# Optimization experiments

Hardware: AMD Instinct MI355X
Metric: run time of the kernel (lower is better)

Reference implementation:

```python
import jax, jax.numpy as jnp
import numpy as np

B, S, D, H, HD = 1, 2048, 1024, 16, 64
E, K, F = 8, 2, 2048
Z_COEF, LB_COEF = 0.001, 0.01


def setup_inputs() -> dict:
    key = jax.random.key(0)
    ks = jax.random.split(key, 10)
    s_d = 1.0 / np.sqrt(D)
    s_f = 1.0 / np.sqrt(F)
    return {
        'hidden_states': jax.random.normal(ks[0], (B, S, D), jnp.float32),
        'attention_mask': jnp.tril(jnp.ones((S, S), bool))[None, None],  # causal [1,1,S,S]
        'position_ids': jnp.broadcast_to(jnp.arange(S), (B, S)),
        'ln1_w': jnp.ones((D,), jnp.float32), 'ln1_b': jnp.zeros((D,), jnp.float32),
        'ln2_w': jnp.ones((D,), jnp.float32), 'ln2_b': jnp.zeros((D,), jnp.float32),
        'wq': jax.random.normal(ks[1], (D, D), jnp.float32) * s_d,
        'wk': jax.random.normal(ks[2], (D, D), jnp.float32) * s_d,
        'wv': jax.random.normal(ks[3], (D, D), jnp.float32) * s_d,
        'wo': jax.random.normal(ks[4], (D, D), jnp.float32) * s_d,
        'w_router': jax.random.normal(ks[5], (D, E), jnp.float32) * s_d,
        'w_gate': jax.random.normal(ks[6], (E, D, F), jnp.float32) * s_d,
        'w_up': jax.random.normal(ks[7], (E, D, F), jnp.float32) * s_d,
        'w_down': jax.random.normal(ks[8], (E, F, D), jnp.float32) * s_f,
    }


def _layernorm(x, w, b):
    m = x.mean(-1, keepdims=True)
    v = jnp.mean(jnp.square(x - m), -1, keepdims=True)
    return (x - m) / jnp.sqrt(v + 1e-5) * w + b


def _rotate_half(x):
    x1, x2 = jnp.split(x, 2, axis=-1)
    return jnp.concatenate([-x2, x1], axis=-1)


def _forward(hs, mask, pos, l1w, l1b, l2w, l2b, wq, wk, wv, wo, wr, wg, wu, wd):
    b, s, d = hs.shape
    # --- attention sub-block ---
    res = hs
    x = _layernorm(hs, l1w, l1b)
    q = (x @ wq).reshape(b, s, H, HD).transpose(0, 2, 1, 3)  # [b,H,s,hd]
    k = (x @ wk).reshape(b, s, H, HD).transpose(0, 2, 1, 3)
    v = (x @ wv).reshape(b, s, H, HD).transpose(0, 2, 1, 3)
    inv_freq = 1.0 / (10000.0 ** (jnp.arange(0, HD, 2, dtype=jnp.float32) / HD))
    freqs = pos[..., None].astype(jnp.float32) * inv_freq  # [b,s,hd/2]
    cos = jnp.cos(freqs); sin = jnp.sin(freqs)
    cos = jnp.concatenate([cos, cos], -1)[:, None]  # [b,1,s,hd]
    sin = jnp.concatenate([sin, sin], -1)[:, None]
    q = q * cos + _rotate_half(q) * sin
    k = k * cos + _rotate_half(k) * sin
    scores = jnp.einsum('bhqd,bhkd->bhqk', q, k) / np.sqrt(HD)
    scores = jnp.where(mask, scores, jnp.asarray(-1e9, scores.dtype))
    attn_w = jax.nn.softmax(scores, axis=-1)
    a = jnp.einsum('bhqk,bhkd->bhqd', attn_w, v)
    a = a.transpose(0, 2, 1, 3).reshape(b, s, d)
    hs = res + a @ wo
    # --- MoE sub-block ---
    res = hs
    x = _layernorm(hs, l2w, l2b)
    xt = x.reshape(-1, d)  # [T,D]
    logits = xt @ wr  # [T,E]
    probs = jax.nn.softmax(logits.astype(jnp.float32), axis=-1)
    ew, ei = jax.lax.top_k(probs, K)  # [T,K]
    ew = ew / ew.sum(-1, keepdims=True)
    one_hot = jax.nn.one_hot(ei, E, dtype=jnp.float32)  # [T,K,E]
    combine = jnp.sum(one_hot * ew[..., None], axis=1).astype(xt.dtype)  # [T,E]
    g = jnp.einsum('td,edf->etf', xt, wg)
    u = jnp.einsum('td,edf->etf', xt, wu)
    y = jnp.einsum('etf,efd->etd', jax.nn.silu(g) * u, wd)  # [E,T,D]
    moe_out = jnp.einsum('te,etd->td', combine, y).reshape(b, s, d)
    # --- aux losses ---
    z_loss = Z_COEF * jnp.mean(jnp.square(jax.scipy.special.logsumexp(logits, axis=-1)))
    expert_mask = jnp.sum(one_hot, axis=1)  # [T,E] in {0,1}
    util = expert_mask.sum(0) / (b * s)
    lb_loss = LB_COEF * jnp.sum(util * probs.mean(0))
    aux = z_loss + lb_loss
    return res + moe_out, aux


def reference(hidden_states, attention_mask, position_ids, ln1_w, ln1_b, ln2_w, ln2_b,
              wq, wk, wv, wo, w_router, w_gate, w_up, w_down):
    return _forward(hidden_states, attention_mask, position_ids, ln1_w, ln1_b, ln2_w, ln2_b,
                    wq, wk, wv, wo, w_router, w_gate, w_up, w_down)
```

## Files before the change

### kernel.cpp

```cpp
#include <hip/hip_runtime.h>
#include <math.h>

static constexpr int S = 2048;
static constexpr int D = 1024;
static constexpr int H = 16;
static constexpr int HD = 64;
static constexpr int E = 8;
static constexpr int F = 2048;
static constexpr int NSLOTS = S * 2;
static constexpr int NPAD = NSLOTS + 128;

typedef __attribute__((ext_vector_type(8))) short bf16x8;
typedef __attribute__((ext_vector_type(4))) float f32x4;

__device__ __forceinline__ float bf2f(ushort u) {
    uint32_t x = ((uint32_t)u) << 16; float f; __builtin_memcpy(&f, &x, 4); return f;
}
__device__ __forceinline__ ushort f2bf(float f) {
    uint32_t x; __builtin_memcpy(&x, &f, 4);
    return (ushort)((x + 0x7fffu + ((x >> 16) & 1u)) >> 16);
}
__device__ __forceinline__ void async_copy16(const void* gptr, void* ldsptr) {
    __builtin_amdgcn_global_load_lds(
        (const __attribute__((address_space(1))) void*)gptr,
        (__attribute__((address_space(3))) void*)ldsptr, 16, 0, 0);
}

__global__ __launch_bounds__(256) void castT_kernel(const float* __restrict__ src,
    ushort* __restrict__ dst, int K, int N)
{
    __shared__ float T[64][65];
    int z = blockIdx.z;
    src += (size_t)z * K * N; dst += (size_t)z * K * N;
    int k0 = blockIdx.y * 64, n0 = blockIdx.x * 64;
    int t = threadIdx.x;
    int r = t >> 4, c4 = (t & 15) * 4;
#pragma unroll
    for (int it = 0; it < 4; it++) {
        float4 v = *(const float4*)(src + (size_t)(k0 + r + it * 16) * N + n0 + c4);
        T[r + it * 16][c4 + 0] = v.x; T[r + it * 16][c4 + 1] = v.y;
        T[r + it * 16][c4 + 2] = v.z; T[r + it * 16][c4 + 3] = v.w;
    }
    __syncthreads();
#pragma unroll
    for (int it = 0; it < 4; it++) {
        int rr = r + it * 16;
        ushort4 o;
        o.x = f2bf(T[c4 + 0][rr]); o.y = f2bf(T[c4 + 1][rr]);
        o.z = f2bf(T[c4 + 2][rr]); o.w = f2bf(T[c4 + 3][rr]);
        *(ushort4*)(dst + (size_t)(n0 + rr) * K + k0 + c4) = o;
    }
}

__global__ __launch_bounds__(256) void castT2_kernel(const float* __restrict__ src,
    ushort* __restrict__ dh, ushort* __restrict__ dl, int K, int N)
{
    __shared__ float T[64][65];
    src += (size_t)blockIdx.z * K * N;
    dh += (size_t)blockIdx.z * K * N; dl += (size_t)blockIdx.z * K * N;
    int k0 = blockIdx.y * 64, n0 = blockIdx.x * 64;
    int t = threadIdx.x;
    int r = t >> 4, c4 = (t & 15) * 4;
#pragma unroll
    for (int it = 0; it < 4; it++) {
        float4 v = *(const float4*)(src + (size_t)(k0 + r + it * 16) * N + n0 + c4);
        T[r + it * 16][c4 + 0] = v.x; T[r + it * 16][c4 + 1] = v.y;
        T[r + it * 16][c4 + 2] = v.z; T[r + it * 16][c4 + 3] = v.w;
    }
    __syncthreads();
#pragma unroll
    for (int it = 0; it < 4; it++) {
        int rr = r + it * 16;
        ushort4 oh, ol;
        float v0 = T[c4 + 0][rr], v1 = T[c4 + 1][rr], v2 = T[c4 + 2][rr], v3 = T[c4 + 3][rr];
        oh.x = f2bf(v0); ol.x = f2bf(v0 - bf2f(oh.x));
        oh.y = f2bf(v1); ol.y = f2bf(v1 - bf2f(oh.y));
        oh.z = f2bf(v2); ol.z = f2bf(v2 - bf2f(oh.z));
        oh.w = f2bf(v3); ol.w = f2bf(v3 - bf2f(oh.w));
        *(ushort4*)(dh + (size_t)(n0 + rr) * K + k0 + c4) = oh;
        *(ushort4*)(dl + (size_t)(n0 + rr) * K + k0 + c4) = ol;
    }
}

__global__ __launch_bounds__(256) void ln_kernel(const float* __restrict__ x,
    const float* __restrict__ w, const float* __restrict__ b,
    float* __restrict__ yf, ushort* __restrict__ yh, ushort* __restrict__ yl)
{
    int t = blockIdx.x, tid = threadIdx.x;
    __shared__ float redx[256];
    __shared__ float redy[256];
    const float* xr = x + (size_t)t * D;
    float4 xv = *(const float4*)(xr + tid * 4);
    redx[tid] = xv.x + xv.y + xv.z + xv.w;
    redy[tid] = xv.x * xv.x + xv.y * xv.y + xv.z * xv.z + xv.w * xv.w;
    __syncthreads();
    for (int st = 128; st > 0; st >>= 1) {
        if (tid < st) { redx[tid] += redx[tid + st]; redy[tid] += redy[tid + st]; }
        __syncthreads();
    }
    float mean = redx[0] * (1.0f / D);
    float var  = redy[0] * (1.0f / D) - mean * mean;
    float rstd = rsqrtf(var + 1e-5f);
    float4 wv = *(const float4*)(w + tid * 4);
    float4 bv = *(const float4*)(b + tid * 4);
    float4 o;
    o.x = (xv.x - mean) * rstd * wv.x + bv.x;
    o.y = (xv.y - mean) * rstd * wv.y + bv.y;
    o.z = (xv.z - mean) * rstd * wv.z + bv.z;
    o.w = (xv.w - mean) * rstd * wv.w + bv.w;
    if (yf) *(float4*)(yf + (size_t)t * D + tid * 4) = o;
    ushort4 oh;
    oh.x = f2bf(o.x); oh.y = f2bf(o.y); oh.z = f2bf(o.z); oh.w = f2bf(o.w);
    if (yh) *(ushort4*)(yh + (size_t)t * D + tid * 4) = oh;
    if (yl) {
        ushort4 ol;
        ol.x = f2bf(o.x - bf2f(oh.x)); ol.y = f2bf(o.y - bf2f(oh.y));
        ol.z = f2bf(o.z - bf2f(oh.z)); ol.w = f2bf(o.w - bf2f(oh.w));
        *(ushort4*)(yl + (size_t)t * D + tid * 4) = ol;
    }
}

__global__ __launch_bounds__(512) void rope_cast(const float* __restrict__ q,
    const float* __restrict__ k, ushort* __restrict__ qh, ushort* __restrict__ ql,
    ushort* __restrict__ kh, ushort* __restrict__ kl)
{
    int t = blockIdx.x;
    int idx = threadIdx.x;
    int hh = idx >> 5, i = idx & 31;
    float invf = powf(10000.0f, -(float)i / 32.0f);
    float ang = (float)t * invf;
    float cc = cosf(ang), ss = sinf(ang);
    size_t base = (size_t)t * D + hh * HD + i;
    const float QS = 0.125f * 1.4426950408889634f;
    float q1 = q[base], q2 = q[base + 32];
    float qr1 = (q1 * cc - q2 * ss) * QS;
    float qr2 = (q2 * cc + q1 * ss) * QS;
    ushort h1 = f2bf(qr1); qh[base] = h1;      ql[base] = f2bf(qr1 - bf2f(h1));
    ushort h2 = f2bf(qr2); qh[base + 32] = h2; ql[base + 32] = f2bf(qr2 - bf2f(h2));
    float k1 = k[base], k2 = k[base + 32];
    float kr1 = k1 * cc - k2 * ss;
    float kr2 = k2 * cc + k1 * ss;
    ushort h3 = f2bf(kr1); kh[base] = h3;      kl[base] = f2bf(kr1 - bf2f(h3));
    ushort h4 = f2bf(kr2); kh[base + 32] = h4; kl[base + 32] = f2bf(kr2 - bf2f(h4));
}

__device__ __forceinline__ void mfma2_kloop(const ushort* __restrict__ Ah_g,
    const ushort* __restrict__ Al_g, const ushort* __restrict__ Bh_g,
    const ushort* __restrict__ Bl_g, int lda, int ldb, int K,
    ushort* sAh, ushort* sAl, ushort* sBh, ushort* sBl, f32x4 (&acc)[4][4])
{
    const int tid = threadIdx.x;
    const int w = tid >> 6, l = tid & 63;
    const int wm = (w >> 1) * 64, wn = (w & 1) * 64;
    const int kc = l >> 4, lr = l & 15;
    for (int k0 = 0; k0 < K; k0 += 32) {
#pragma unroll
        for (int it = 0; it < 2; it++) {
            int c = it * 256 + tid;
            int ckc = c >> 7, r = c & 127;
            int loff = (it * 256 + w * 64) * 8;
            size_t ga = (size_t)r * lda + k0 + ckc * 8;
            size_t gb = (size_t)r * ldb + k0 + ckc * 8;
            async_copy16(Ah_g + ga, sAh + loff);
            async_copy16(Al_g + ga, sAl + loff);
            async_copy16(Bh_g + gb, sBh + loff);
            async_copy16(Bl_g + gb, sBl + loff);
        }
        __syncthreads();
        bf16x8 ah[4], al[4], bh[4], bl[4];
#pragma unroll
        for (int f = 0; f < 4; f++) {
            int ao = (kc * 128 + wm + f * 16 + lr) * 8;
            int bo = (kc * 128 + wn + f * 16 + lr) * 8;
            ah[f] = *(const bf16x8*)(sAh + ao);
            al[f] = *(const bf16x8*)(sAl + ao);
            bh[f] = *(const bf16x8*)(sBh + bo);
            bl[f] = *(const bf16x8*)(sBl + bo);
        }
#pragma unroll
        for (int fm = 0; fm < 4; fm++)
#pragma unroll
            for (int fn = 0; fn < 4; fn++) {
                acc[fm][fn] = __builtin_amdgcn_mfma_f32_16x16x32_bf16(ah[fm], bh[fn], acc[fm][fn], 0, 0, 0);
                acc[fm][fn] = __builtin_amdgcn_mfma_f32_16x16x32_bf16(ah[fm], bl[fn], acc[fm][fn], 0, 0, 0);
                acc[fm][fn] = __builtin_amdgcn_mfma_f32_16x16x32_bf16(al[fm], bh[fn], acc[fm][fn], 0, 0, 0);
            }
        __syncthreads();
    }
}

__global__ __launch_bounds__(256) void qkv_mfma2(const ushort* __restrict__ xh,
    const ushort* __restrict__ xl,
    const ushort* __restrict__ wqh, const ushort* __restrict__ wql,
    const ushort* __restrict__ wkh, const ushort* __restrict__ wkl,
    const ushort* __restrict__ wvh, const ushort* __restrict__ wvl,
    float* __restrict__ qo, float* __restrict__ ko, float* __restrict__ vo)
{
    __shared__ ushort sAh[4096], sAl[4096], sBh[4096], sBl[4096];
    const ushort* Bh = blockIdx.z == 0 ? wqh : (blockIdx.z == 1 ? wkh : wvh);
    const ushort* Bl = blockIdx.z == 0 ? wql : (blockIdx.z == 1 ? wkl : wvl);
    float* C = blockIdx.z == 0 ? qo : (blockIdx.z == 1 ? ko : vo);
    int m0 = blockIdx.y * 128, n0 = blockIdx.x * 128;
    f32x4 acc[4][4];
#pragma unroll
    for (int i = 0; i < 4; i++)
#pragma unroll
        for (int j = 0; j < 4; j++) acc[i][j] = (f32x4){0.f, 0.f, 0.f, 0.f};
    mfma2_kloop(xh + (size_t)m0 * D, xl + (size_t)m0 * D,
                Bh + (size_t)n0 * D, Bl + (size_t)n0 * D, D, D, D,
                sAh, sAl, sBh, sBl, acc);
    const int l = threadIdx.x & 63, w = threadIdx.x >> 6;
    const int wm = (w >> 1) * 64, wn = (w & 1) * 64;
#pragma unroll
    for (int fm = 0; fm < 4; fm++)
#pragma unroll
        for (int fn = 0; fn < 4; fn++)
#pragma unroll
            for (int r = 0; r < 4; r++) {
                int row = m0 + wm + fm * 16 + (l >> 4) * 4 + r;
                int col = n0 + wn + fn * 16 + (l & 15);
                C[(size_t)row * D + col] = acc[fm][fn][r];
            }
}

__global__ __launch_bounds__(256) void wo_mfma2(const ushort* __restrict__ ah,
    const ushort* __restrict__ al, const ushort* __restrict__ wh, const ushort* __restrict__ wl,
    const float* __restrict__ resid, float* __restrict__ Cout)
{
    __shared__ ushort sAh[4096], sAl[4096], sBh[4096], sBl[4096];
    int m0 = blockIdx.y * 128, n0 = blockIdx.x * 128;
    f32x4 acc[4][4];
#pragma unroll
    for (int i = 0; i < 4; i++)
#pragma unroll
        for (int j = 0; j < 4; j++) acc[i][j] = (f32x4){0.f, 0.f, 0.f, 0.f};
    mfma2_kloop(ah + (size_t)m0 * D, al + (size_t)m0 * D,
                wh + (size_t)n0 * D, wl + (size_t)n0 * D, D, D, D,
                sAh, sAl, sBh, sBl, acc);
    const int l = threadIdx.x & 63, w = threadIdx.x >> 6;
    const int wm = (w >> 1) * 64, wn = (w & 1) * 64;
#pragma unroll
    for (int fm = 0; fm < 4; fm++)
#pragma unroll
        for (int fn = 0; fn < 4; fn++)
#pragma unroll
            for (int r = 0; r < 4; r++) {
                int row = m0 + wm + fm * 16 + (l >> 4) * 4 + r;
                int col = n0 + wn + fn * 16 + (l & 15);
                Cout[(size_t)row * D + col] = acc[fm][fn][r] + resid[(size_t)row * D + col];
            }
}

__global__ __launch_bounds__(256) void attn_mfma(
    const ushort* __restrict__ qhp, const ushort* __restrict__ qlp,
    const ushort* __restrict__ khp, const ushort* __restrict__ klp,
    const ushort* __restrict__ vth, const ushort* __restrict__ vtl,
    ushort* __restrict__ oh_out, ushort* __restrict__ ol_out)
{
    __shared__ ushort sK[2][2][4096];
    __shared__ ushort sV[2][2][4096];
    __shared__ ushort sP[4][2][1024];
    const int h = blockIdx.y;
    const int tid = threadIdx.x;
    const int w = tid >> 6, l = tid & 63;
    const int g = l >> 4, c = l & 15;
    const size_t hoff = (size_t)h * HD;
    ushort* sPh = &sP[w][0][0];
    ushort* sPl = &sP[w][1][0];

#define STAGE_KV(buf, kt_)                                                        \
  do {                                                                            \
    const int k0s = (kt_) * 64;                                                   \
    int cb0 = w * 64;                                                             \
    int ch0 = cb0 + l;                                                            \
    size_t kg0 = (size_t)(k0s + (ch0 & 63)) * D + hoff + (ch0 >> 6) * 8;          \
    size_t vg0 = (hoff + (ch0 & 63)) * (size_t)S + k0s + (ch0 >> 6) * 8;          \
    async_copy16(khp + kg0, &sK[buf][0][cb0 * 8]);                                \
    async_copy16(klp + kg0, &sK[buf][1][cb0 * 8]);                                \
    async_copy16(vth + vg0, &sV[buf][0][cb0 * 8]);                                \
    async_copy16(vtl + vg0, &sV[buf][1][cb0 * 8]);                                \
    int cb1 = 256 + w * 64;                                                       \
    int ch1 = cb1 + l;                                                            \
    size_t kg1 = (size_t)(k0s + (ch1 & 63)) * D + hoff + (ch1 >> 6) * 8;          \
    size_t vg1 = (hoff + (ch1 & 63)) * (size_t)S + k0s + (ch1 >> 6) * 8;          \
    async_copy16(khp + kg1, &sK[buf][0][cb1 * 8]);                                \
    async_copy16(klp + kg1, &sK[buf][1][cb1 * 8]);                                \
    async_copy16(vth + vg1, &sV[buf][0][cb1 * 8]);                                \
    async_copy16(vtl + vg1, &sV[buf][1][cb1 * 8]);                                \
  } while (0)

    for (int half = 0; half < 2; half++) {
        const int qt = (half == 0) ? (int)blockIdx.x : 31 - (int)blockIdx.x;
        const size_t qrow = (size_t)(qt * 64 + w * 16 + c) * D + hoff;
        bf16x8 aqh0 = *(const bf16x8*)(qhp + qrow + g * 8);
        bf16x8 aqh1 = *(const bf16x8*)(qhp + qrow + 32 + g * 8);
        bf16x8 aql0 = *(const bf16x8*)(qlp + qrow + g * 8);
        bf16x8 aql1 = *(const bf16x8*)(qlp + qrow + 32 + g * 8);

        STAGE_KV(0, 0);
        asm volatile("s_waitcnt vmcnt(0)" ::: "memory");
        __builtin_amdgcn_s_barrier();
        __builtin_amdgcn_sched_barrier(0);

        float m_[4], l_[4];
        f32x4 oacc[4];
#pragma unroll
        for (int r = 0; r < 4; r++) { m_[r] = -3e38f; l_[r] = 0.0f; }
#pragma unroll
        for (int fn = 0; fn < 4; fn++) oacc[fn] = (f32x4){0.f, 0.f, 0.f, 0.f};

        for (int kt = 0; kt <= qt; kt++) {
            const int cur = kt & 1;
            if (kt < qt) STAGE_KV(1 - cur, kt + 1);
            const ushort* sKh = &sK[cur][0][0];
            const ushort* sKl = &sK[cur][1][0];
            bf16x8 b0[4], b1[4], c0[4], c1[4];
#pragma unroll
            for (int fn = 0; fn < 4; fn++) {
                int u0 = (g * 64 + fn * 16 + c) * 8;
                int u1 = ((4 + g) * 64 + fn * 16 + c) * 8;
                b0[fn] = *(const bf16x8*)(sKh + u0);
                b1[fn] = *(const bf16x8*)(sKh + u1);
                c0[fn] = *(const bf16x8*)(sKl + u0);
                c1[fn] = *(const bf16x8*)(sKl + u1);
            }
            f32x4 sacc[4];
#pragma unroll
            for (int fn = 0; fn < 4; fn++) {
                f32x4 a = (f32x4){0.f, 0.f, 0.f, 0.f};
                a = __builtin_amdgcn_mfma_f32_16x16x32_bf16(aqh0, b0[fn], a, 0, 0, 0);
                a = __builtin_amdgcn_mfma_f32_16x16x32_bf16(aqh1, b1[fn], a, 0, 0, 0);
                a = __builtin_amdgcn_mfma_f32_16x16x32_bf16(aqh0, c0[fn], a, 0, 0, 0);
                a = __builtin_amdgcn_mfma_f32_16x16x32_bf16(aqh1, c1[fn], a, 0, 0, 0);
                a = __builtin_amdgcn_mfma_f32_16x16x32_bf16(aql0, b0[fn], a, 0, 0, 0);
                a = __builtin_amdgcn_mfma_f32_16x16x32_bf16(aql1, b1[fn], a, 0, 0, 0);
                sacc[fn] = a;
            }
            if (kt == qt) {
#pragma unroll
                for (int fn = 0; fn < 4; fn++)
#pragma unroll
                    for (int r = 0; r < 4; r++)
                        if (fn * 16 + c > w * 16 + g * 4 + r) sacc[fn][r] = -3e38f;
            }
            float alpha[4];
#pragma unroll
            for (int r = 0; r < 4; r++) {
                float rm = fmaxf(fmaxf(sacc[0][r], sacc[1][r]), fmaxf(sacc[2][r], sacc[3][r]));
#pragma unroll
                for (int off = 1; off < 16; off <<= 1) rm = fmaxf(rm, __shfl_xor(rm, off));
                float mn = fmaxf(m_[r], rm);
                alpha[r] = exp2f(m_[r] - mn);
                m_[r] = mn;
                float rs = 0.0f;
#pragma unroll
                for (int fn = 0; fn < 4; fn++) {
                    float pp = exp2f(sacc[fn][r] - mn);
                    sacc[fn][r] = pp;
                    rs += pp;
                }
#pragma unroll
                for (int off = 1; off < 16; off <<= 1) rs += __shfl_xor(rs, off);
                l_[r] = l_[r] * alpha[r] + rs;
            }
#pragma unroll
            for (int fn = 0; fn < 4; fn++)
#pragma unroll
                for (int r = 0; r < 4; r++) oacc[fn][r] *= alpha[r];
#pragma unroll
            for (int fn = 0; fn < 4; fn++) {
                int chunk = fn * 2 + (c >> 3);
#pragma unroll
                for (int r = 0; r < 4; r++) {
                    float pp = sacc[fn][r];
                    ushort ph = f2bf(pp);
                    int off = (chunk * 16 + g * 4 + r) * 8 + (c & 7);
                    sPh[off] = ph;
                    sPl[off] = f2bf(pp - bf2f(ph));
                }
            }
            const ushort* sVh = &sV[cur][0][0];
            const ushort* sVl = &sV[cur][1][0];
            bf16x8 pa0 = *(const bf16x8*)(sPh + (g * 16 + c) * 8);
            bf16x8 pa1 = *(const bf16x8*)(sPh + ((4 + g) * 16 + c) * 8);
            bf16x8 pb0 = *(const bf16x8*)(sPl + (g * 16 + c) * 8);
            bf16x8 pb1 = *(const bf16x8*)(sPl + ((4 + g) * 16 + c) * 8);
#pragma unroll
            for (int fn = 0; fn < 4; fn++) {
                int u0 = (g * 64 + fn * 16 + c) * 8;
                int u1 = ((4 + g) * 64 + fn * 16 + c) * 8;
                bf16x8 vh0 = *(const bf16x8*)(sVh + u0);
                bf16x8 vh1 = *(const bf16x8*)(sVh + u1);
                bf16x8 vl0 = *(const bf16x8*)(sVl + u0);
                bf16x8 vl1 = *(const bf16x8*)(sVl + u1);
                f32x4 o = oacc[fn];
                o = __builtin_amdgcn_mfma_f32_16x16x32_bf16(pa0, vh0, o, 0, 0, 0);
                o = __builtin_amdgcn_mfma_f32_16x16x32_bf16(pa1, vh1, o, 0, 0, 0);
                o = __builtin_amdgcn_mfma_f32_16x16x32_bf16(pa0, vl0, o, 0, 0, 0);
                o = __builtin_amdgcn_mfma_f32_16x16x32_bf16(pa1, vl1, o, 0, 0, 0);
                o = __builtin_amdgcn_mfma_f32_16x16x32_bf16(pb0, vh0, o, 0, 0, 0);
                o = __builtin_amdgcn_mfma_f32_16x16x32_bf16(pb1, vh1, o, 0, 0, 0);
                oacc[fn] = o;
            }
            if (kt < qt) {
                asm volatile("s_waitcnt vmcnt(0)" ::: "memory");
                __builtin_amdgcn_s_barrier();
                __builtin_amdgcn_sched_barrier(0);
            }
        }
#pragma unroll
        for (int r = 0; r < 4; r++) {
            float inv = 1.0f / l_[r];
            size_t orow = (size_t)(qt * 64 + w * 16 + g * 4 + r) * D + hoff;
#pragma unroll
            for (int fn = 0; fn < 4; fn++) {
                float v = oacc[fn][r] * inv;
                ushort hi = f2bf(v);
                oh_out[orow + fn * 16 + c] = hi;
                ol_out[orow + fn * 16 + c] = f2bf(v - bf2f(hi));
            }
        }
        __syncthreads();
    }
#undef STAGE_KV
}

__global__ __launch_bounds__(64) void router_kernel(const float* __restrict__ x,
    const float* __restrict__ wr, int* __restrict__ ei, float* __restrict__ ew,
    int* __restrict__ counts, float* __restrict__ prob_sums, float* __restrict__ z_sum)
{
    int t = blockIdx.x, lane = threadIdx.x;
    const float* xr = x + (size_t)t * D;
    float p[E] = {};
    for (int d = lane; d < D; d += 64) {
        float xd = xr[d];
        const float* wrow = wr + d * E;
#pragma unroll
        for (int e = 0; e < E; e++) p[e] = fmaf(xd, wrow[e], p[e]);
    }
#pragma unroll
    for (int off = 32; off > 0; off >>= 1) {
#pragma unroll
        for (int e = 0; e < E; e++) p[e] += __shfl_xor(p[e], off);
    }
    float m = p[0];
#pragma unroll
    for (int e = 1; e < E; e++) m = fmaxf(m, p[e]);
    float sum = 0.0f, pr[E];
#pragma unroll
    for (int e = 0; e < E; e++) { pr[e] = expf(p[e] - m); sum += pr[e]; }
    float invs = 1.0f / sum;
#pragma unroll
    for (int e = 0; e < E; e++) pr[e] *= invs;
    float lse = m + logf(sum);
    int e1 = 0; float b1 = pr[0];
#pragma unroll
    for (int e = 1; e < E; e++) if (pr[e] > b1) { b1 = pr[e]; e1 = e; }
    int e2 = -1; float b2 = -1.0f;
#pragma unroll
    for (int e = 0; e < E; e++) if (e != e1 && pr[e] > b2) { b2 = pr[e]; e2 = e; }
    float wsum = b1 + b2;
    if (lane == 0) {
        ei[2 * t] = e1; ei[2 * t + 1] = e2;
        ew[2 * t] = b1 / wsum; ew[2 * t + 1] = b2 / wsum;
        atomicAdd(&counts[e1], 1);
        atomicAdd(&counts[e2], 1);
        atomicAdd(z_sum, lse * lse);
    }
    if (lane < E) atomicAdd(&prob_sums[lane], pr[lane]);
}

__global__ void zero_kernel(int* counts, float* prob_sums, float* z_sum)
{
    int tid = threadIdx.x;
    if (tid < E) { counts[tid] = 0; prob_sums[tid] = 0.0f; }
    if (tid == 0) *z_sum = 0.0f;
}

__global__ void finalize_kernel(const int* __restrict__ counts, const float* __restrict__ prob_sums,
    const float* __restrict__ z_sum, int* __restrict__ offs, int* __restrict__ cursor,
    float* __restrict__ aux_out)
{
    if (threadIdx.x == 0) {
        int off = 0;
        for (int e = 0; e < E; e++) { offs[e] = off; cursor[e] = off; off += counts[e]; }
        float z = 1e-3f * (*z_sum) * (1.0f / S);
        float lb = 0.0f;
        for (int e = 0; e < E; e++) lb += ((float)counts[e] / (float)S) * (prob_sums[e] / (float)S);
        lb *= 1e-2f;
        *aux_out = z + lb;
    }
}

__global__ __launch_bounds__(256) void scatter_kernel(const int* __restrict__ ei,
    int* __restrict__ cursor, int* __restrict__ tlist, int* __restrict__ slot_of)
{
    int t = blockIdx.x * 256 + threadIdx.x;
    if (t >= S) return;
#pragma unroll
    for (int kk = 0; kk < 2; kk++) {
        int e = ei[2 * t + kk];
        int slot = atomicAdd(&cursor[e], 1);
        tlist[slot] = t;
        slot_of[2 * t + kk] = slot;
    }
}

__global__ __launch_bounds__(256) void gather_kernel(const ushort* __restrict__ xbf,
    const int* __restrict__ tlist, ushort* __restrict__ xg)
{
    int slot = blockIdx.x;
    int t4 = threadIdx.x * 4;
    ushort4 vv;
    if (slot < NSLOTS) {
        int tok = tlist[slot];
        vv = *(const ushort4*)(xbf + (size_t)tok * D + t4);
    } else {
        vv = make_ushort4(0, 0, 0, 0);
    }
    *(ushort4*)(xg + (size_t)slot * D + t4) = vv;
}

__global__ __launch_bounds__(256) void moe_gateup_mfma(const ushort* __restrict__ xg,
    const ushort* __restrict__ wgt, const ushort* __restrict__ wut,
    ushort* __restrict__ Hb, const int* __restrict__ offs, const int* __restrict__ cnts)
{
    int e = blockIdx.z;
    int cnt = cnts[e];
    int m0 = blockIdx.y * 128;
    if (m0 >= cnt) return;
    int off = offs[e];
    const ushort* Gt = wgt + (size_t)e * F * D;
    const ushort* Ut = wut + (size_t)e * F * D;
    int n0 = blockIdx.x * 128;
    __shared__ ushort As[8192], Gs[8192], Us[8192];
    const int tid = threadIdx.x;
    const int w = tid >> 6, l = tid & 63;
    const int wm = (w >> 1) * 64, wn = (w & 1) * 64;
    const ushort* Arow = xg + (size_t)(off + m0) * D;
    const ushort* Grow = Gt + (size_t)n0 * D;
    const ushort* Urow = Ut + (size_t)n0 * D;
    f32x4 accg[4][4], accu[4][4];
#pragma unroll
    for (int i = 0; i < 4; i++)
#pragma unroll
        for (int j = 0; j < 4; j++) { accg[i][j] = (f32x4){0.f,0.f,0.f,0.f}; accu[i][j] = (f32x4){0.f,0.f,0.f,0.f}; }
    for (int k0 = 0; k0 < D; k0 += 64) {
#pragma unroll
        for (int it = 0; it < 4; it++) {
            int c = it * 256 + tid;
            int kc = c >> 7, r = c & 127;
            async_copy16(Arow + (size_t)r * D + k0 + kc * 8, As + (size_t)(it * 256 + w * 64) * 8);
            async_copy16(Grow + (size_t)r * D + k0 + kc * 8, Gs + (size_t)(it * 256 + w * 64) * 8);
            async_copy16(Urow + (size_t)r * D + k0 + kc * 8, Us + (size_t)(it * 256 + w * 64) * 8);
        }
        __syncthreads();
#pragma unroll
        for (int hh = 0; hh < 2; hh++) {
            bf16x8 af[4], gf[4], uf[4];
            int kc = hh * 4 + (l >> 4);
#pragma unroll
            for (int f = 0; f < 4; f++) {
                af[f] = *(const bf16x8*)(As + (size_t)(kc * 128 + wm + f * 16 + (l & 15)) * 8);
                gf[f] = *(const bf16x8*)(Gs + (size_t)(kc * 128 + wn + f * 16 + (l & 15)) * 8);
                uf[f] = *(const bf16x8*)(Us + (size_t)(kc * 128 + wn + f * 16 + (l & 15)) * 8);
            }
#pragma unroll
            for (int fm = 0; fm < 4; fm++)
#pragma unroll
                for (int fn = 0; fn < 4; fn++) {
                    accg[fm][fn] = __builtin_amdgcn_mfma_f32_16x16x32_bf16(af[fm], gf[fn], accg[fm][fn], 0, 0, 0);
                    accu[fm][fn] = __builtin_amdgcn_mfma_f32_16x16x32_bf16(af[fm], uf[fn], accu[fm][fn], 0, 0, 0);
                }
        }
        __syncthreads();
    }
#pragma unroll
    for (int fm = 0; fm < 4; fm++)
#pragma unroll
        for (int fn = 0; fn < 4; fn++)
#pragma unroll
            for (int r = 0; r < 4; r++) {
                int rloc = m0 + wm + fm * 16 + (l >> 4) * 4 + r;
                if (rloc < cnt) {
                    int col = n0 + wn + fn * 16 + (l & 15);
                    float g = accg[fm][fn][r], u = accu[fm][fn][r];
                    Hb[(size_t)(off + rloc) * F + col] = f2bf(g / (1.0f + expf(-g)) * u);
                }
            }
}

__global__ __launch_bounds__(256) void moe_down_mfma(const ushort* __restrict__ Hb,
    const ushort* __restrict__ wdt, ushort* __restrict__ yb,
    const int* __restrict__ offs, const int* __restrict__ cnts)
{
    int e = blockIdx.z;
    int cnt = cnts[e];
    int m0 = blockIdx.y * 128;
    if (m0 >= cnt) return;
    int off = offs[e];
    const ushort* Bt = wdt + (size_t)e * D * F;
    int n0 = blockIdx.x * 128;
    __shared__ ushort As[8192], Bs[8192];
    const int tid = threadIdx.x;
    const int w = tid >> 6, l = tid & 63;
    const int wm = (w >> 1) * 64, wn = (w & 1) * 64;
    const ushort* Arow = Hb + (size_t)(off + m0) * F;
    const ushort* Brow = Bt + (size_t)n0 * F;
    f32x4 acc[4][4];
#pragma unroll
    for (int i = 0; i < 4; i++)
#pragma unroll
        for (int j = 0; j < 4; j++) acc[i][j] = (f32x4){0.f,0.f,0.f,0.f};
    for (int k0 = 0; k0 < F; k0 += 64) {
#pragma unroll
        for (int it = 0; it < 4; it++) {
            int c = it * 256 + tid;
            int kc = c >> 7, r = c & 127;
            async_copy16(Arow + (size_t)r * F + k0 + kc * 8, As + (size_t)(it * 256 + w * 64) * 8);
            async_copy16(Brow + (size_t)r * F + k0 + kc * 8, Bs + (size_t)(it * 256 + w * 64) * 8);
        }
        __syncthreads();
#pragma unroll
        for (int hh = 0; hh < 2; hh++) {
            bf16x8 af[4], bfr[4];
            int kc = hh * 4 + (l >> 4);
#pragma unroll
            for (int f = 0; f < 4; f++) {
                af[f]  = *(const bf16x8*)(As + (size_t)(kc * 128 + wm + f * 16 + (l & 15)) * 8);
                bfr[f] = *(const bf16x8*)(Bs + (size_t)(kc * 128 + wn + f * 16 + (l & 15)) * 8);
            }
#pragma unroll
            for (int fm = 0; fm < 4; fm++)
#pragma unroll
                for (int fn = 0; fn < 4; fn++)
                    acc[fm][fn] = __builtin_amdgcn_mfma_f32_16x16x32_bf16(af[fm], bfr[fn], acc[fm][fn], 0, 0, 0);
        }
        __syncthreads();
    }
#pragma unroll
    for (int fm = 0; fm < 4; fm++)
#pragma unroll
        for (int fn = 0; fn < 4; fn++)
#pragma unroll
            for (int r = 0; r < 4; r++) {
                int rloc = m0 + wm + fm * 16 + (l >> 4) * 4 + r;
                if (rloc < cnt) {
                    int col = n0 + wn + fn * 16 + (l & 15);
                    yb[(size_t)(off + rloc) * D + col] = f2bf(acc[fm][fn][r]);
                }
            }
}

__global__ __launch_bounds__(256) void combine_kernel(const float* __restrict__ hs2,
    const ushort* __restrict__ yb, const float* __restrict__ ew,
    const int* __restrict__ slot_of, float* __restrict__ out)
{
    int t = blockIdx.x, tid = threadIdx.x;
    int s0 = slot_of[2 * t], s1 = slot_of[2 * t + 1];
    float w0 = ew[2 * t], w1 = ew[2 * t + 1];
    float4 a = *(const float4*)(hs2 + (size_t)t * D + tid * 4);
    ushort4 y0 = *(const ushort4*)(yb + (size_t)s0 * D + tid * 4);
    ushort4 y1 = *(const ushort4*)(yb + (size_t)s1 * D + tid * 4);
    float4 o;
    o.x = a.x + w0 * bf2f(y0.x) + w1 * bf2f(y1.x);
    o.y = a.y + w0 * bf2f(y0.y) + w1 * bf2f(y1.y);
    o.z = a.z + w0 * bf2f(y0.z) + w1 * bf2f(y1.z);
    o.w = a.w + w0 * bf2f(y0.w) + w1 * bf2f(y1.w);
    *(float4*)(out + (size_t)t * D + tid * 4) = o;
}

extern "C" void kernel_launch(void* const* d_in, const int* in_sizes, int n_in,
                              void* d_out, int out_size, void* d_ws, size_t ws_size,
                              hipStream_t stream)
{
    (void)in_sizes; (void)n_in; (void)out_size; (void)ws_size;
    const float* hs   = (const float*)d_in[0];
    const float* ln1w = (const float*)d_in[3];
    const float* ln1b = (const float*)d_in[4];
    const float* ln2w = (const float*)d_in[5];
    const float* ln2b = (const float*)d_in[6];
    const float* wq   = (const float*)d_in[7];
    const float* wk   = (const float*)d_in[8];
    const float* wv   = (const float*)d_in[9];
    const float* wo   = (const float*)d_in[10];
    const float* wr   = (const float*)d_in[11];
    const float* wg   = (const float*)d_in[12];
    const float* wu   = (const float*)d_in[13];
    const float* wd   = (const float*)d_in[14];
    float* out = (float*)d_out;

    const size_t TD = (size_t)S * D;
    char* p = (char*)d_ws;
    auto alloc = [&](size_t bytes) { char* r = p; p += (bytes + 255) & ~(size_t)255; return r; };

    ushort* wgt  = (ushort*)alloc((size_t)E * D * F * 2);
    ushort* wut  = (ushort*)alloc((size_t)E * D * F * 2);
    ushort* wdt  = (ushort*)alloc((size_t)E * D * F * 2);
    ushort* wqh  = (ushort*)alloc((size_t)D * D * 2);
    ushort* wqlo = (ushort*)alloc((size_t)D * D * 2);
    ushort* wkh  = (ushort*)alloc((size_t)D * D * 2);
    ushort* wklo = (ushort*)alloc((size_t)D * D * 2);
    ushort* wvh  = (ushort*)alloc((size_t)D * D * 2);
    ushort* wvlo = (ushort*)alloc((size_t)D * D * 2);
    ushort* woh  = (ushort*)alloc((size_t)D * D * 2);
    ushort* wolo = (ushort*)alloc((size_t)D * D * 2);
    ushort* xh   = (ushort*)alloc(TD * 2);
    ushort* xl   = (ushort*)alloc(TD * 2);
    float*  qb   = (float*)alloc(TD * 4);
    float*  kb   = (float*)alloc(TD * 4);
    float*  vb   = (float*)alloc(TD * 4);
    ushort* ath  = (ushort*)alloc(TD * 2);
    ushort* atl  = (ushort*)alloc(TD * 2);
    float*  hs2  = (float*)alloc(TD * 4);
    float*  xf32 = (float*)alloc(TD * 4);
    ushort* xbf  = (ushort*)alloc(TD * 2);
    ushort* xg   = (ushort*)alloc((size_t)NPAD * D * 2);
    ushort* Hb   = (ushort*)alloc((size_t)NPAD * F * 2);
    ushort* yb   = (ushort*)alloc((size_t)NPAD * D * 2);
    ushort* khp  = (ushort*)alloc(TD * 2);
    ushort* klp  = (ushort*)alloc(TD * 2);
    ushort* vth  = (ushort*)alloc(TD * 2);
    ushort* vtl  = (ushort*)alloc(TD * 2);
    float*  ewb       = (float*)alloc(2 * S * 4);
    float*  prob_sums = (float*)alloc(8 * 4);
    float*  z_sum     = (float*)alloc(8 * 4);
    int* ei      = (int*)alloc(2 * S * 4);
    int* slot_of = (int*)alloc(2 * S * 4);
    int* tlist   = (int*)alloc(NSLOTS * 4);
    int* counts  = (int*)alloc(8 * 4);
    int* offs    = (int*)alloc(8 * 4);
    int* cursor  = (int*)alloc(8 * 4);

    castT2_kernel<<<dim3(D / 64, D / 64, 1), 256, 0, stream>>>(wq, wqh, wqlo, D, D);
    castT2_kernel<<<dim3(D / 64, D / 64, 1), 256, 0, stream>>>(wk, wkh, wklo, D, D);
    castT2_kernel<<<dim3(D / 64, D / 64, 1), 256, 0, stream>>>(wv, wvh, wvlo, D, D);
    castT2_kernel<<<dim3(D / 64, D / 64, 1), 256, 0, stream>>>(wo, woh, wolo, D, D);
    castT_kernel<<<dim3(F / 64, D / 64, E), 256, 0, stream>>>(wg, wgt, D, F);
    castT_kernel<<<dim3(F / 64, D / 64, E), 256, 0, stream>>>(wu, wut, D, F);
    castT_kernel<<<dim3(D / 64, F / 64, E), 256, 0, stream>>>(wd, wdt, F, D);

    ln_kernel<<<S, 256, 0, stream>>>(hs, ln1w, ln1b, nullptr, xh, xl);
    qkv_mfma2<<<dim3(D / 128, S / 128, 3), 256, 0, stream>>>(xh, xl, wqh, wqlo, wkh, wklo, wvh, wvlo, qb, kb, vb);
    rope_cast<<<S, 512, 0, stream>>>(qb, kb, xh, xl, khp, klp);
    castT2_kernel<<<dim3(D / 64, S / 64, 1), 256, 0, stream>>>(vb, vth, vtl, S, D);
    attn_mfma<<<dim3(16, H), 256, 0, stream>>>(xh, xl, khp, klp, vth, vtl, ath, atl);
    wo_mfma2<<<dim3(D / 128, S / 128), 256, 0, stream>>>(ath, atl, woh, wolo, hs, hs2);

    ln_kernel<<<S, 256, 0, stream>>>(hs2, ln2w, ln2b, xf32, xbf, nullptr);
    zero_kernel<<<1, 64, 0, stream>>>(counts, prob_sums, z_sum);
    router_kernel<<<S, 64, 0, stream>>>(xf32, wr, ei, ewb, counts, prob_sums, z_sum);
    finalize_kernel<<<1, 64, 0, stream>>>(counts, prob_sums, z_sum, offs, cursor, out + TD);
    scatter_kernel<<<S / 256, 256, 0, stream>>>(ei, cursor, tlist, slot_of);
    gather_kernel<<<NPAD, 256, 0, stream>>>(xbf, tlist, xg);
    moe_gateup_mfma<<<dim3(F / 128, NSLOTS / 128, E), 256, 0, stream>>>(xg, wgt, wut, Hb, offs, counts);
    moe_down_mfma<<<dim3(D / 128, NSLOTS / 128, E), 256, 0, stream>>>(Hb, wdt, yb, offs, counts);
    combine_kernel<<<S, 256, 0, stream>>>(hs2, yb, ewb, slot_of, out);
}
```

Before: 899.5 us.

## Software-pipeline GEMM k-loops with multi-buffered LDS and split MoE gate/up

The split-bf16 GEMM k-loop now double-buffers LDS, and the MoE gate/up and down kernels triple-buffer their LDS tiles. Each loop issues the next tile's async global-to-LDS copies before computing on the current one, using vmcnt waits and one barrier per step instead of two syncthreads. Gate and up projections become separate column blocks of one launch writing bf16 outputs into reused q/v buffers, with a new silu kernel combining them. This targets load latency and raises the block count, but adds an extra pass over the intermediate activations, extra bf16 rounding before SiLU, and larger LDS footprints that may lower occupancy.

```diff
diff --git a/kernel.cpp b/kernel.cpp
--- a/kernel.cpp
+++ b/kernel.cpp
@@ -144,38 +144,54 @@
     ushort h4 = f2bf(kr2); kh[base + 32] = h4; kl[base + 32] = f2bf(kr2 - bf2f(h4));
 }
 
+__device__ __forceinline__ void stage_m2(const ushort* __restrict__ Ah_g,
+    const ushort* __restrict__ Al_g, const ushort* __restrict__ Bh_g,
+    const ushort* __restrict__ Bl_g, int lda, int ldb, int kbase,
+    ushort* sAh, ushort* sAl, ushort* sBh, ushort* sBl, int tid, int w)
+{
+#pragma unroll
+    for (int it = 0; it < 2; it++) {
+        int c = it * 256 + tid;
+        int ckc = c >> 7, r = c & 127;
+        int loff = (it * 256 + w * 64) * 8;
+        size_t ga = (size_t)r * lda + kbase + ckc * 8;
+        size_t gb = (size_t)r * ldb + kbase + ckc * 8;
+        async_copy16(Ah_g + ga, sAh + loff);
+        async_copy16(Al_g + ga, sAl + loff);
+        async_copy16(Bh_g + gb, sBh + loff);
+        async_copy16(Bl_g + gb, sBl + loff);
+    }
+}
+
 __device__ __forceinline__ void mfma2_kloop(const ushort* __restrict__ Ah_g,
     const ushort* __restrict__ Al_g, const ushort* __restrict__ Bh_g,
     const ushort* __restrict__ Bl_g, int lda, int ldb, int K,
-    ushort* sAh, ushort* sAl, ushort* sBh, ushort* sBl, f32x4 (&acc)[4][4])
+    ushort (&sAh)[2][4096], ushort (&sAl)[2][4096],
+    ushort (&sBh)[2][4096], ushort (&sBl)[2][4096], f32x4 (&acc)[4][4])
 {
     const int tid = threadIdx.x;
     const int w = tid >> 6, l = tid & 63;
     const int wm = (w >> 1) * 64, wn = (w & 1) * 64;
     const int kc = l >> 4, lr = l & 15;
-    for (int k0 = 0; k0 < K; k0 += 32) {
-#pragma unroll
-        for (int it = 0; it < 2; it++) {
-            int c = it * 256 + tid;
-            int ckc = c >> 7, r = c & 127;
-            int loff = (it * 256 + w * 64) * 8;
-            size_t ga = (size_t)r * lda + k0 + ckc * 8;
-            size_t gb = (size_t)r * ldb + k0 + ckc * 8;
-            async_copy16(Ah_g + ga, sAh + loff);
-            async_copy16(Al_g + ga, sAl + loff);
-            async_copy16(Bh_g + gb, sBh + loff);
-            async_copy16(Bl_g + gb, sBl + loff);
-        }
-        __syncthreads();
+    const int NT = K / 32;
+    stage_m2(Ah_g, Al_g, Bh_g, Bl_g, lda, ldb, 0, sAh[0], sAl[0], sBh[0], sBl[0], tid, w);
+    for (int t = 0; t < NT; ++t) {
+        const int cur = t & 1;
+        asm volatile("s_waitcnt vmcnt(0)" ::: "memory");
+        __builtin_amdgcn_s_barrier();
+        __builtin_amdgcn_sched_barrier(0);
+        if (t + 1 < NT)
+            stage_m2(Ah_g, Al_g, Bh_g, Bl_g, lda, ldb, (t + 1) * 32,
+                     sAh[1 - cur], sAl[1 - cur], sBh[1 - cur], sBl[1 - cur], tid, w);
         bf16x8 ah[4], al[4], bh[4], bl[4];
 #pragma unroll
         for (int f = 0; f < 4; f++) {
             int ao = (kc * 128 + wm + f * 16 + lr) * 8;
             int bo = (kc * 128 + wn + f * 16 + lr) * 8;
-            ah[f] = *(const bf16x8*)(sAh + ao);
-            al[f] = *(const bf16x8*)(sAl + ao);
-            bh[f] = *(const bf16x8*)(sBh + bo);
-            bl[f] = *(const bf16x8*)(sBl + bo);
+            ah[f] = *(const bf16x8*)(sAh[cur] + ao);
+            al[f] = *(const bf16x8*)(sAl[cur] + ao);
+            bh[f] = *(const bf16x8*)(sBh[cur] + bo);
+            bl[f] = *(const bf16x8*)(sBl[cur] + bo);
         }
 #pragma unroll
         for (int fm = 0; fm < 4; fm++)
@@ -185,7 +201,6 @@
                 acc[fm][fn] = __builtin_amdgcn_mfma_f32_16x16x32_bf16(ah[fm], bl[fn], acc[fm][fn], 0, 0, 0);
                 acc[fm][fn] = __builtin_amdgcn_mfma_f32_16x16x32_bf16(al[fm], bh[fn], acc[fm][fn], 0, 0, 0);
             }
-        __syncthreads();
     }
 }
 
@@ -196,7 +211,7 @@
     const ushort* __restrict__ wvh, const ushort* __restrict__ wvl,
     float* __restrict__ qo, float* __restrict__ ko, float* __restrict__ vo)
 {
-    __shared__ ushort sAh[4096], sAl[4096], sBh[4096], sBl[4096];
+    __shared__ ushort sAh[2][4096], sAl[2][4096], sBh[2][4096], sBl[2][4096];
     const ushort* Bh = blockIdx.z == 0 ? wqh : (blockIdx.z == 1 ? wkh : wvh);
     const ushort* Bl = blockIdx.z == 0 ? wql : (blockIdx.z == 1 ? wkl : wvl);
     float* C = blockIdx.z == 0 ? qo : (blockIdx.z == 1 ? ko : vo);
@@ -227,7 +242,7 @@
     const ushort* __restrict__ al, const ushort* __restrict__ wh, const ushort* __restrict__ wl,
     const float* __restrict__ resid, float* __restrict__ Cout)
 {
-    __shared__ ushort sAh[4096], sAl[4096], sBh[4096], sBl[4096];
+    __shared__ ushort sAh[2][4096], sAl[2][4096], sBh[2][4096], sBl[2][4096];
     int m0 = blockIdx.y * 128, n0 = blockIdx.x * 128;
     f32x4 acc[4][4];
 #pragma unroll
@@ -523,58 +538,69 @@
 
 __global__ __launch_bounds__(256) void moe_gateup_mfma(const ushort* __restrict__ xg,
     const ushort* __restrict__ wgt, const ushort* __restrict__ wut,
-    ushort* __restrict__ Hb, const int* __restrict__ offs, const int* __restrict__ cnts)
-{
-    int e = blockIdx.z;
-    int cnt = cnts[e];
-    int m0 = blockIdx.y * 128;
+    ushort* __restrict__ Hg, ushort* __restrict__ Hu,
+    const int* __restrict__ offs, const int* __restrict__ cnts)
+{
+    const int e = blockIdx.z;
+    const int cnt = cnts[e];
+    const int m0 = blockIdx.y * 128;
     if (m0 >= cnt) return;
-    int off = offs[e];
-    const ushort* Gt = wgt + (size_t)e * F * D;
-    const ushort* Ut = wut + (size_t)e * F * D;
-    int n0 = blockIdx.x * 128;
-    __shared__ ushort As[8192], Gs[8192], Us[8192];
+    const int off = offs[e];
+    const int n0g = blockIdx.x * 128;
+    const bool isg = n0g < F;
+    const ushort* Wt = isg ? (wgt + (size_t)e * F * D + (size_t)n0g * D)
+                           : (wut + (size_t)e * F * D + (size_t)(n0g - F) * D);
+    ushort* Outp = isg ? Hg : Hu;
+    const int ncol0 = isg ? n0g : n0g - F;
+    __shared__ ushort As[3][4096], Ws[3][4096];
     const int tid = threadIdx.x;
     const int w = tid >> 6, l = tid & 63;
     const int wm = (w >> 1) * 64, wn = (w & 1) * 64;
+    const int kc = l >> 4, lr = l & 15;
     const ushort* Arow = xg + (size_t)(off + m0) * D;
-    const ushort* Grow = Gt + (size_t)n0 * D;
-    const ushort* Urow = Ut + (size_t)n0 * D;
-    f32x4 accg[4][4], accu[4][4];
+
+#define STAGE_GU(buf, t_)                                                     \
+  do {                                                                        \
+    int kbase = (t_) * 32;                                                    \
+    _Pragma("unroll")                                                         \
+    for (int it = 0; it < 2; it++) {                                          \
+      int cch = it * 256 + tid;                                               \
+      int ckc = cch >> 7, r = cch & 127;                                      \
+      int loff = (it * 256 + w * 64) * 8;                                     \
+      async_copy16(Arow + (size_t)r * D + kbase + ckc * 8, As[buf] + loff);   \
+      async_copy16(Wt   + (size_t)r * D + kbase + ckc * 8, Ws[buf] + loff);   \
+    }                                                                         \
+  } while (0)
+
+    f32x4 acc[4][4];
 #pragma unroll
     for (int i = 0; i < 4; i++)
 #pragma unroll
-        for (int j = 0; j < 4; j++) { accg[i][j] = (f32x4){0.f,0.f,0.f,0.f}; accu[i][j] = (f32x4){0.f,0.f,0.f,0.f}; }
-    for (int k0 = 0; k0 < D; k0 += 64) {
-#pragma unroll
-        for (int it = 0; it < 4; it++) {
-            int c = it * 256 + tid;
-            int kc = c >> 7, r = c & 127;
-            async_copy16(Arow + (size_t)r * D + k0 + kc * 8, As + (size_t)(it * 256 + w * 64) * 8);
-            async_copy16(Grow + (size_t)r * D + k0 + kc * 8, Gs + (size_t)(it * 256 + w * 64) * 8);
-            async_copy16(Urow + (size_t)r * D + k0 + kc * 8, Us + (size_t)(it * 256 + w * 64) * 8);
+        for (int j = 0; j < 4; j++) acc[i][j] = (f32x4){0.f, 0.f, 0.f, 0.f};
+
+    const int NT = D / 32;
+    STAGE_GU(0, 0);
+    STAGE_GU(1, 1);
+    for (int t = 0; t < NT; ++t) {
+        const int cur = t % 3;
+        if (t + 1 < NT) { asm volatile("s_waitcnt vmcnt(4)" ::: "memory"); }
+        else            { asm volatile("s_waitcnt vmcnt(0)" ::: "memory"); }
+        __builtin_amdgcn_s_barrier();
+        __builtin_amdgcn_sched_barrier(0);
+        if (t + 2 < NT) STAGE_GU((t + 2) % 3, t + 2);
+        bf16x8 af[4], wf[4];
+#pragma unroll
+        for (int f = 0; f < 4; f++) {
+            af[f] = *(const bf16x8*)(As[cur] + (kc * 128 + wm + f * 16 + lr) * 8);
+            wf[f] = *(const bf16x8*)(Ws[cur] + (kc * 128 + wn + f * 16 + lr) * 8);
         }
-        __syncthreads();
-#pragma unroll
-        for (int hh = 0; hh < 2; hh++) {
-            bf16x8 af[4], gf[4], uf[4];
-            int kc = hh * 4 + (l >> 4);
-#pragma unroll
-            for (int f = 0; f < 4; f++) {
-                af[f] = *(const bf16x8*)(As + (size_t)(kc * 128 + wm + f * 16 + (l & 15)) * 8);
-                gf[f] = *(const bf16x8*)(Gs + (size_t)(kc * 128 + wn + f * 16 + (l & 15)) * 8);
-                uf[f] = *(const bf16x8*)(Us + (size_t)(kc * 128 + wn + f * 16 + (l & 15)) * 8);
-            }
-#pragma unroll
-            for (int fm = 0; fm < 4; fm++)
-#pragma unroll
-                for (int fn = 0; fn < 4; fn++) {
-                    accg[fm][fn] = __builtin_amdgcn_mfma_f32_16x16x32_bf16(af[fm], gf[fn], accg[fm][fn], 0, 0, 0);
-                    accu[fm][fn] = __builtin_amdgcn_mfma_f32_16x16x32_bf16(af[fm], uf[fn], accu[fm][fn], 0, 0, 0);
-                }
-        }
-        __syncthreads();
-    }
+#pragma unroll
+        for (int fm = 0; fm < 4; fm++)
+#pragma unroll
+            for (int fn = 0; fn < 4; fn++)
+                acc[fm][fn] = __builtin_amdgcn_mfma_f32_16x16x32_bf16(af[fm], wf[fn], acc[fm][fn], 0, 0, 0);
+    }
+#undef STAGE_GU
 #pragma unroll
     for (int fm = 0; fm < 4; fm++)
 #pragma unroll
@@ -583,61 +609,90 @@
             for (int r = 0; r < 4; r++) {
                 int rloc = m0 + wm + fm * 16 + (l >> 4) * 4 + r;
                 if (rloc < cnt) {
-                    int col = n0 + wn + fn * 16 + (l & 15);
-                    float g = accg[fm][fn][r], u = accu[fm][fn][r];
-                    Hb[(size_t)(off + rloc) * F + col] = f2bf(g / (1.0f + expf(-g)) * u);
+                    int col = ncol0 + wn + fn * 16 + (l & 15);
+                    Outp[(size_t)(off + rloc) * F + col] = f2bf(acc[fm][fn][r]);
                 }
             }
+}
+
+__global__ __launch_bounds__(256) void silu_kernel(const ushort* __restrict__ Gout,
+    const ushort* __restrict__ Uout, ushort* __restrict__ Hb)
+{
+    int slot = blockIdx.x;
+    int f0 = threadIdx.x * 8;
+    bf16x8 gv = *(const bf16x8*)(Gout + (size_t)slot * F + f0);
+    bf16x8 uv = *(const bf16x8*)(Uout + (size_t)slot * F + f0);
+    bf16x8 o;
+#pragma unroll
+    for (int j = 0; j < 8; j++) {
+        float g = bf2f((ushort)gv[j]);
+        float u = bf2f((ushort)uv[j]);
+        o[j] = (short)f2bf(g / (1.0f + expf(-g)) * u);
+    }
+    *(bf16x8*)(Hb + (size_t)slot * F + f0) = o;
 }
 
 __global__ __launch_bounds__(256) void moe_down_mfma(const ushort* __restrict__ Hb,
     const ushort* __restrict__ wdt, ushort* __restrict__ yb,
     const int* __restrict__ offs, const int* __restrict__ cnts)
 {
-    int e = blockIdx.z;
-    int cnt = cnts[e];
-    int m0 = blockIdx.y * 128;
+    const int e = blockIdx.z;
+    const int cnt = cnts[e];
+    const int m0 = blockIdx.y * 128;
     if (m0 >= cnt) return;
-    int off = offs[e];
+    const int off = offs[e];
     const ushort* Bt = wdt + (size_t)e * D * F;
-    int n0 = blockIdx.x * 128;
-    __shared__ ushort As[8192], Bs[8192];
+    const int n0 = blockIdx.x * 128;
+    __shared__ ushort As[3][4096], Bs[3][4096];
     const int tid = threadIdx.x;
     const int w = tid >> 6, l = tid & 63;
     const int wm = (w >> 1) * 64, wn = (w & 1) * 64;
+    const int kc = l >> 4, lr = l & 15;
     const ushort* Arow = Hb + (size_t)(off + m0) * F;
     const ushort* Brow = Bt + (size_t)n0 * F;
+
+#define STAGE_DN(buf, t_)                                                     \
+  do {                                                                        \
+    int kbase = (t_) * 32;                                                    \
+    _Pragma("unroll")                                                         \
+    for (int it = 0; it < 2; it++) {                                          \
+      int cch = it * 256 + tid;                                               \
+      int ckc = cch >> 7, r = cch & 127;                                      \
+      int loff = (it * 256 + w * 64) * 8;                                     \
+      async_copy16(Arow + (size_t)r * F + kbase + ckc * 8, As[buf] + loff);   \
+      async_copy16(Brow + (size_t)r * F + kbase + ckc * 8, Bs[buf] + loff);   \
+    }                                                                         \
+  } while (0)
+
     f32x4 acc[4][4];
 #pragma unroll
     for (int i = 0; i < 4; i++)
 #pragma unroll
-        for (int j = 0; j < 4; j++) acc[i][j] = (f32x4){0.f,0.f,0.f,0.f};
-    for (int k0 = 0; k0 < F; k0 += 64) {
-#pragma unroll
-        for (int it = 0; it < 4; it++) {
-            int c = it * 256 + tid;
-            int kc = c >> 7, r = c & 127;
-            async_copy16(Arow + (size_t)r * F + k0 + kc * 8, As + (size_t)(it * 256 + w * 64) * 8);
-            async_copy16(Brow + (size_t)r * F + k0 + kc * 8, Bs + (size_t)(it * 256 + w * 64) * 8);
+        for (int j = 0; j < 4; j++) acc[i][j] = (f32x4){0.f, 0.f, 0.f, 0.f};
+
+    const int NT = F / 32;
+    STAGE_DN(0, 0);
+    STAGE_DN(1, 1);
+    for (int t = 0; t < NT; ++t) {
+        const int cur = t % 3;
+        if (t + 1 < NT) { asm volatile("s_waitcnt vmcnt(4)" ::: "memory"); }
+        else            { asm volatile("s_waitcnt vmcnt(0)" ::: "memory"); }
+        __builtin_amdgcn_s_barrier();
+        __builtin_amdgcn_sched_barrier(0);
+        if (t + 2 < NT) STAGE_DN((t + 2) % 3, t + 2);
+        bf16x8 af[4], bfr[4];
+#pragma unroll
+        for (int f = 0; f < 4; f++) {
+            af[f]  = *(const bf16x8*)(As[cur] + (kc * 128 + wm + f * 16 + lr) * 8);
+            bfr[f] = *(const bf16x8*)(Bs[cur] + (kc * 128 + wn + f * 16 + lr) * 8);
         }
-        __syncthreads();
-#pragma unroll
-        for (int hh = 0; hh < 2; hh++) {
-            bf16x8 af[4], bfr[4];
-            int kc = hh * 4 + (l >> 4);
-#pragma unroll
-            for (int f = 0; f < 4; f++) {
-                af[f]  = *(const bf16x8*)(As + (size_t)(kc * 128 + wm + f * 16 + (l & 15)) * 8);
-                bfr[f] = *(const bf16x8*)(Bs + (size_t)(kc * 128 + wn + f * 16 + (l & 15)) * 8);
-            }
-#pragma unroll
-            for (int fm = 0; fm < 4; fm++)
-#pragma unroll
-                for (int fn = 0; fn < 4; fn++)
-                    acc[fm][fn] = __builtin_amdgcn_mfma_f32_16x16x32_bf16(af[fm], bfr[fn], acc[fm][fn], 0, 0, 0);
-        }
-        __syncthreads();
-    }
+#pragma unroll
+        for (int fm = 0; fm < 4; fm++)
+#pragma unroll
+            for (int fn = 0; fn < 4; fn++)
+                acc[fm][fn] = __builtin_amdgcn_mfma_f32_16x16x32_bf16(af[fm], bfr[fn], acc[fm][fn], 0, 0, 0);
+    }
+#undef STAGE_DN
 #pragma unroll
     for (int fm = 0; fm < 4; fm++)
 #pragma unroll
@@ -732,6 +787,9 @@
     int* offs    = (int*)alloc(8 * 4);
     int* cursor  = (int*)alloc(8 * 4);
 
+    ushort* Gout = (ushort*)qb;
+    ushort* Uout = (ushort*)vb;
+
     castT2_kernel<<<dim3(D / 64, D / 64, 1), 256, 0, stream>>>(wq, wqh, wqlo, D, D);
     castT2_kernel<<<dim3(D / 64, D / 64, 1), 256, 0, stream>>>(wk, wkh, wklo, D, D);
     castT2_kernel<<<dim3(D / 64, D / 64, 1), 256, 0, stream>>>(wv, wvh, wvlo, D, D);
@@ -753,7 +811,8 @@
     finalize_kernel<<<1, 64, 0, stream>>>(counts, prob_sums, z_sum, offs, cursor, out + TD);
     scatter_kernel<<<S / 256, 256, 0, stream>>>(ei, cursor, tlist, slot_of);
     gather_kernel<<<NPAD, 256, 0, stream>>>(xbf, tlist, xg);
-    moe_gateup_mfma<<<dim3(F / 128, NSLOTS / 128, E), 256, 0, stream>>>(xg, wgt, wut, Hb, offs, counts);
+    moe_gateup_mfma<<<dim3(2 * F / 128, NSLOTS / 128, E), 256, 0, stream>>>(xg, wgt, wut, Gout, Uout, offs, counts);
+    silu_kernel<<<NSLOTS, 256, 0, stream>>>(Gout, Uout, Hb);
     moe_down_mfma<<<dim3(D / 128, NSLOTS / 128, E), 256, 0, stream>>>(Hb, wdt, yb, offs, counts);
     combine_kernel<<<S, 256, 0, stream>>>(hs2, yb, ewb, slot_of, out);
 }
```

After: 868.6 us. 1.04x faster.
